# Optimization experiments

Hardware: AMD Instinct MI355X
Metric: run time of the kernel (lower is better)

## Reference

```python
import jax, jax.numpy as jnp
import numpy as np

SP = 4
HEADS = 4
LN_EPS = 1e-4


def _branch(q, k, v, h, hsp, w, wsp, lepe_w, lepe_b, scale, heads):
    # q,k,v: [B, L, Cb] with spatial layout (h hsp w wsp), channel layout (c head)
    B = q.shape[0]
    Cb = q.shape[-1]
    c = Cb // heads

    def win(t):
        t = t.reshape(B, h, hsp, w, wsp, c, heads)
        t = t.transpose(0, 1, 3, 6, 2, 4, 5)  # B,h,w,head,hsp,wsp,c
        return t.reshape(B * h * w, heads, hsp * wsp, c)

    q, k, v = win(q), win(k), win(v)
    Bw = B * h * w
    # LePE: depthwise 3x3 conv on v in image layout [(b h w), (c head), hsp, wsp]
    vimg = v.reshape(Bw, heads, hsp, wsp, c).transpose(0, 4, 1, 2, 3).reshape(Bw, Cb, hsp, wsp)
    lepe = jax.lax.conv_general_dilated(
        vimg, lepe_w, window_strides=(1, 1), padding='SAME',
        dimension_numbers=('NCHW', 'OIHW', 'NCHW'), feature_group_count=Cb)
    lepe = lepe + lepe_b[None, :, None, None]
    lepe = lepe.reshape(Bw, c, heads, hsp, wsp).transpose(0, 2, 3, 4, 1).reshape(Bw, heads, hsp * wsp, c)
    # stripe-window attention
    attn = jax.nn.softmax((q * scale) @ jnp.swapaxes(k, -2, -1), axis=-1)
    o = attn @ v + lepe
    # back to image: [(b h w), head, (hsp wsp), c] -> [B, (c head), (h hsp), (w wsp)]
    o = o.reshape(B, h, w, heads, hsp, wsp, c).transpose(0, 6, 3, 1, 4, 2, 5)
    o = o.reshape(B, Cb, h * hsp, w * wsp)
    return o, attn


def reference(x, ln_g, ln_b, w_qkv, proj_w, proj_b, lepe_w1, lepe_b1, lepe_w2, lepe_b2):
    B, C, H, W = x.shape
    heads, sp = HEADS, SP
    scale = (C // heads) ** (-0.5)  # scale uses full dim // num_heads as in __init__
    # [B,C,H,W] -> [B, H*W, C], LayerNorm over C
    xp = x.transpose(0, 2, 3, 1).reshape(B, H * W, C)
    mu = xp.mean(-1, keepdims=True)
    var = xp.var(-1, keepdims=True)
    xn = (xp - mu) * jax.lax.rsqrt(var + LN_EPS) * ln_g + ln_b
    qkv = xn @ w_qkv.T  # [B, L, 3C]
    q, k, v = jnp.split(qkv, 3, axis=-1)
    Ch = C // 2
    # branch 1: vertical stripes (full H, width sp); branch 2: horizontal stripes
    params = [(1, H, W // sp, sp, lepe_w1, lepe_b1),
              (H // sp, sp, 1, W, lepe_w2, lepe_b2)]
    outs, attns = [], []
    for i, (h, hsp, w, wsp, lw, lb) in enumerate(params):
        sl = slice(i * Ch, (i + 1) * Ch)
        o, a = _branch(q[..., sl], k[..., sl], v[..., sl], h, hsp, w, wsp, lw, lb, scale, heads)
        outs.append(o)
        attns.append(a)
    xcat = jnp.concatenate(outs, axis=1)  # [B, C, H, W]
    out = jnp.einsum('bchw,oc->bohw', xcat, proj_w[:, :, 0, 0]) + proj_b[None, :, None, None]
    return (out, attns[0], attns[1])


def setup_inputs() -> dict:
    key = jax.random.key(0)
    ks = jax.random.split(key, 6)
    B, C, H, W = 8, 256, 64, 64
    return {
        'x': jax.random.normal(ks[0], (B, C, H, W), dtype=jnp.float32),
        'ln_g': jnp.ones((C,), jnp.float32),
        'ln_b': jnp.zeros((C,), jnp.float32),
        'w_qkv': jax.random.normal(ks[1], (3 * C, C), dtype=jnp.float32) * 0.02,
        'proj_w': jax.random.normal(ks[2], (C, C, 1, 1), dtype=jnp.float32) * 0.02,
        'proj_b': jnp.zeros((C,), jnp.float32),
        'lepe_w1': jax.random.normal(ks[3], (C // 2, 1, 3, 3), dtype=jnp.float32) * 0.1,
        'lepe_b1': jnp.zeros((C // 2,), jnp.float32),
        'lepe_w2': jax.random.normal(ks[4], (C // 2, 1, 3, 3), dtype=jnp.float32) * 0.1,
        'lepe_b2': jnp.zeros((C // 2,), jnp.float32),
    }
```

## Files before the change

kernel.cpp:

```cpp
#include <hip/hip_runtime.h>
#include <math.h>

typedef short bf8 __attribute__((ext_vector_type(8)));
typedef float f4  __attribute__((ext_vector_type(4)));

__device__ inline float b2f(unsigned short u) {
    return __uint_as_float(((unsigned int)u) << 16);
}
__device__ inline unsigned short f2b(float f) {
    unsigned int u = __float_as_uint(f);
    u = (u + 0x7fffu + ((u >> 16) & 1u)) >> 16;
    return (unsigned short)u;
}

__global__ __launch_bounds__(256) void k_ln_t(const float* __restrict__ x,
                                              const float* __restrict__ g,
                                              const float* __restrict__ beta,
                                              unsigned short* __restrict__ xnb) {
    __shared__ float xt[32 * 261];
    __shared__ float ps[8][32];
    __shared__ float ps2[8][32];
    __shared__ float ms[32];
    __shared__ float rs[32];
    int l0 = blockIdx.x * 32, b = blockIdx.y;
    int tid = threadIdx.x;
    int tl = tid & 31, c0 = tid >> 5;
    const float* xb = x + (size_t)b * 1048576 + l0 + tl;
    float s = 0.f, s2 = 0.f;
#pragma unroll 8
    for (int rr = 0; rr < 32; ++rr) {
        int c = rr * 8 + c0;
        float v = xb[(size_t)c * 4096];
        int cm = c ^ (((rr >> 2) & 7) << 2);
        xt[tl * 261 + cm] = v;
        s += v; s2 += v * v;
    }
    ps[c0][tl] = s; ps2[c0][tl] = s2;
    __syncthreads();
    if (tid < 32) {
        float t = 0.f, t2 = 0.f;
#pragma unroll
        for (int j = 0; j < 8; ++j) { t += ps[j][tid]; t2 += ps2[j][tid]; }
        float m = t * (1.f / 256.f);
        float var = t2 * (1.f / 256.f) - m * m;
        ms[tid] = m;
        rs[tid] = rsqrtf(var + 1e-4f);
    }
    __syncthreads();
    int lw = tid >> 3, cc = (tid & 7) * 32;
    int xr = (tid & 7) << 2;
    float m = ms[lw], r = rs[lw];
    unsigned short* dst = xnb + ((size_t)b * 4096 + l0 + lw) * 256 + cc;
#pragma unroll
    for (int q4 = 0; q4 < 4; ++q4) {
        int cb = cc + q4 * 8;
        float gv[8], bv[8];
        *(float4*)(gv)     = *(const float4*)(g + cb);
        *(float4*)(gv + 4) = *(const float4*)(g + cb + 4);
        *(float4*)(bv)     = *(const float4*)(beta + cb);
        *(float4*)(bv + 4) = *(const float4*)(beta + cb + 4);
        union { unsigned short u[8]; uint4 v; } pk;
#pragma unroll
        for (int e = 0; e < 8; ++e) {
            int cm = (cb + e) ^ xr;
            pk.u[e] = f2b((xt[lw * 261 + cm] - m) * r * gv[e] + bv[e]);
        }
        *(uint4*)(dst + q4 * 8) = pk.v;
    }
}

__global__ __launch_bounds__(256) void k_wcvt(const float* __restrict__ w,
                                              unsigned short* __restrict__ wb) {
    int i = (blockIdx.x * 256 + threadIdx.x) * 8;
    float4 a = *(const float4*)(w + i);
    float4 c = *(const float4*)(w + i + 4);
    union { unsigned short u[8]; uint4 v; } r;
    r.u[0] = f2b(a.x); r.u[1] = f2b(a.y); r.u[2] = f2b(a.z); r.u[3] = f2b(a.w);
    r.u[4] = f2b(c.x); r.u[5] = f2b(c.y); r.u[6] = f2b(c.z); r.u[7] = f2b(c.w);
    *(uint4*)(wb + i) = r.v;
}

__global__ __launch_bounds__(256) void k_pcvt(const float* __restrict__ pw,
                                              unsigned short* __restrict__ pwb) {
    int idx = blockIdx.x * 256 + threadIdx.x;
    int o = idx >> 8, cp = idx & 255;
    int br = cp >> 7, head = (cp >> 5) & 3, d = cp & 31;
    int c = br * 128 + d * 4 + head;
    pwb[idx] = f2b(pw[o * 256 + c]);
}

__global__ __launch_bounds__(256) void k_qkv(const unsigned short* __restrict__ wb,
                                             const unsigned short* __restrict__ xnb,
                                             unsigned short* __restrict__ qw,
                                             unsigned short* __restrict__ kw,
                                             unsigned short* __restrict__ vw) {
    int jt = blockIdx.x, lt = blockIdx.y, b = blockIdx.z;
    int tid = threadIdx.x;
    int w = tid >> 6, lane = tid & 63;
    int ln15 = lane & 15, quad = lane >> 4;
    const unsigned short* A = wb + (size_t)jt * 64 * 256 + ln15 * 256 + quad * 8;
    const unsigned short* B = xnb + ((size_t)b * 4096 + lt * 256 + w * 64 + ln15) * 256 + quad * 8;
    const f4 z = {0.f, 0.f, 0.f, 0.f};
    f4 acc[4][4];
#pragma unroll
    for (int i = 0; i < 4; i++)
#pragma unroll
        for (int j = 0; j < 4; j++) acc[i][j] = z;
#pragma unroll 2
    for (int k0 = 0; k0 < 256; k0 += 32) {
        bf8 af[4], bvf[4];
#pragma unroll
        for (int i = 0; i < 4; i++) af[i]  = *(const bf8*)(A + i * 16 * 256 + k0);
#pragma unroll
        for (int j = 0; j < 4; j++) bvf[j] = *(const bf8*)(B + j * 16 * 256 + k0);
#pragma unroll
        for (int i = 0; i < 4; i++)
#pragma unroll
            for (int j = 0; j < 4; j++)
                acc[i][j] = __builtin_amdgcn_mfma_f32_16x16x32_bf16(af[i], bvf[j], acc[i][j], 0, 0, 0);
    }
    int lbase = lt * 256 + w * 64;
#pragma unroll
    for (int i = 0; i < 4; i++) {
#pragma unroll
        for (int r = 0; r < 4; r++) {
            int j = jt * 64 + i * 16 + quad * 4 + r;
            int sel = j >> 8;
            int jr = j & 255;
            int branch = jr >> 7;
            int chb = jr & 127;
            int d = chb >> 2, head = chb & 3;
            unsigned short* dst = (sel == 0) ? qw : ((sel == 1) ? kw : vw);
            float sc = (sel == 0) ? 0.125f : 1.f;
#pragma unroll
            for (int jf = 0; jf < 4; jf++) {
                int ll = lbase + jf * 16 + ln15;
                int row = ll >> 6, col = ll & 63;
                int win, pos;
                if (branch == 0) { win = col >> 2; pos = (row << 2) | (col & 3); }
                else             { win = row >> 2; pos = ((row & 3) << 6) | col; }
                int bw = b * 16 + win;
                size_t idx;
                if (sel == 2)
                    idx = ((((size_t)branch * 128 + bw) * 4 + head) * 32 + d) * 256 + pos;
                else
                    idx = ((((size_t)branch * 128 + bw) * 4 + head) * 256 + pos) * 32 + d;
                dst[idx] = f2b(acc[i][jf][r] * sc);
            }
        }
    }
}

__global__ __launch_bounds__(256, 3) void k_attn(const unsigned short* __restrict__ qw,
                                                 const unsigned short* __restrict__ kw,
                                                 const unsigned short* __restrict__ vw,
                                                 const float* __restrict__ lw1,
                                                 const float* __restrict__ lb1,
                                                 const float* __restrict__ lw2,
                                                 const float* __restrict__ lb2,
                                                 float* __restrict__ attn_out,
                                                 unsigned short* __restrict__ xcat) {
    __shared__ __align__(16) char smem[49792];
    float*          olds = (float*)smem;
    unsigned short* vt   = (unsigned short*)(smem + 32896);

    int bid = blockIdx.x;
    int branch = bid >> 9;
    int bw = (bid >> 2) & 127;
    int head = bid & 3;
    int tid = threadIdx.x;
    int w = tid >> 6, lane = tid & 63;
    int ln15 = lane & 15, quad = lane >> 4;
    int rowbase = w * 64;

    size_t base = (((size_t)branch * 128 + bw) * 4 + head) * 8192;
    const unsigned short* qb = qw + base;
    const unsigned short* kb = kw + base;
    const unsigned short* vb = vw + base;

    {
        int d = tid >> 3, ck = (tid & 7) * 32;
        const uint4* s = (const uint4*)(vb + d * 256 + ck);
        uint4* dst = (uint4*)(vt + d * 264 + ck);
        dst[0] = s[0]; dst[1] = s[1]; dst[2] = s[2]; dst[3] = s[3];
    }

    bf8 qf[4];
#pragma unroll
    for (int rt = 0; rt < 4; rt++)
        qf[rt] = *(const bf8*)(qb + (rowbase + rt * 16 + ln15) * 32 + quad * 8);

    const f4 z = {0.f, 0.f, 0.f, 0.f};

    f4 lsum[4] = {z, z, z, z};
    for (int jtile = 0; jtile < 16; jtile++) {
        bf8 kf = *(const bf8*)(kb + (jtile * 16 + ln15) * 32 + quad * 8);
#pragma unroll
        for (int rt = 0; rt < 4; rt++) {
            f4 s = __builtin_amdgcn_mfma_f32_16x16x32_bf16(qf[rt], kf, z, 0, 0, 0);
            lsum[rt].x += __expf(s.x);
            lsum[rt].y += __expf(s.y);
            lsum[rt].z += __expf(s.z);
            lsum[rt].w += __expf(s.w);
        }
    }
    f4 inv[4];
#pragma unroll
    for (int rt = 0; rt < 4; rt++) {
        float a0 = lsum[rt].x, a1 = lsum[rt].y, a2 = lsum[rt].z, a3 = lsum[rt].w;
#pragma unroll
        for (int m = 1; m < 16; m <<= 1) {
            a0 += __shfl_xor(a0, m); a1 += __shfl_xor(a1, m);
            a2 += __shfl_xor(a2, m); a3 += __shfl_xor(a3, m);
        }
        inv[rt].x = 1.f / a0; inv[rt].y = 1.f / a1;
        inv[rt].z = 1.f / a2; inv[rt].w = 1.f / a3;
    }

    __syncthreads();

    unsigned short* plw = ((unsigned short*)olds) + w * 512;
    float* abase = attn_out + (size_t)branch * 33554432ull
                 + ((size_t)(bw * 4 + head)) * 65536;
    f4 oacc[4][2] = {{z, z}, {z, z}, {z, z}, {z, z}};
    for (int t = 0; t < 8; t++) {
        int c0 = t * 32;
        bf8 kf0 = *(const bf8*)(kb + (c0 + ln15) * 32 + quad * 8);
        bf8 kf1 = *(const bf8*)(kb + (c0 + 16 + ln15) * 32 + quad * 8);
        bf8 vf0 = *(const bf8*)(vt + ln15 * 264 + c0 + quad * 8);
        bf8 vf1 = *(const bf8*)(vt + (16 + ln15) * 264 + c0 + quad * 8);
#pragma unroll
        for (int rt = 0; rt < 4; rt++) {
            f4 s0 = __builtin_amdgcn_mfma_f32_16x16x32_bf16(qf[rt], kf0, z, 0, 0, 0);
            f4 s1 = __builtin_amdgcn_mfma_f32_16x16x32_bf16(qf[rt], kf1, z, 0, 0, 0);
            f4 p0, p1;
            p0.x = __expf(s0.x) * inv[rt].x; p0.y = __expf(s0.y) * inv[rt].y;
            p0.z = __expf(s0.z) * inv[rt].z; p0.w = __expf(s0.w) * inv[rt].w;
            p1.x = __expf(s1.x) * inv[rt].x; p1.y = __expf(s1.y) * inv[rt].y;
            p1.z = __expf(s1.z) * inv[rt].z; p1.w = __expf(s1.w) * inv[rt].w;
            float* ar = abase + (size_t)(rowbase + rt * 16 + quad * 4) * 256 + c0 + ln15;
            ar[0]   = p0.x; ar[256] = p0.y; ar[512] = p0.z; ar[768] = p0.w;
            ar[16]  = p1.x; ar[272] = p1.y; ar[528] = p1.z; ar[784] = p1.w;
            plw[(quad * 4 + 0) * 32 + ln15]      = f2b(p0.x);
            plw[(quad * 4 + 1) * 32 + ln15]      = f2b(p0.y);
            plw[(quad * 4 + 2) * 32 + ln15]      = f2b(p0.z);
            plw[(quad * 4 + 3) * 32 + ln15]      = f2b(p0.w);
            plw[(quad * 4 + 0) * 32 + 16 + ln15] = f2b(p1.x);
            plw[(quad * 4 + 1) * 32 + 16 + ln15] = f2b(p1.y);
            plw[(quad * 4 + 2) * 32 + 16 + ln15] = f2b(p1.z);
            plw[(quad * 4 + 3) * 32 + 16 + ln15] = f2b(p1.w);
            bf8 pf = *(const bf8*)(plw + ln15 * 32 + quad * 8);
            oacc[rt][0] = __builtin_amdgcn_mfma_f32_16x16x32_bf16(pf, vf0, oacc[rt][0], 0, 0, 0);
            oacc[rt][1] = __builtin_amdgcn_mfma_f32_16x16x32_bf16(pf, vf1, oacc[rt][1], 0, 0, 0);
        }
    }

    __syncthreads();
#pragma unroll
    for (int rt = 0; rt < 4; rt++)
#pragma unroll
        for (int dt = 0; dt < 2; dt++) {
            int d = dt * 16 + ln15;
            int r = rowbase + rt * 16 + quad * 4;
            olds[d * 257 + r + 0] = oacc[rt][dt][0];
            olds[d * 257 + r + 1] = oacc[rt][dt][1];
            olds[d * 257 + r + 2] = oacc[rt][dt][2];
            olds[d * 257 + r + 3] = oacc[rt][dt][3];
        }
    __syncthreads();

    const float* lw = branch ? lw2 : lw1;
    const float* lb = branch ? lb2 : lb1;
    int p = tid;
    int hs, ws_;
    if (branch == 0) { hs = p >> 2; ws_ = p & 3; }
    else             { hs = p >> 6; ws_ = p & 63; }
    int win = bw & 15, b = bw >> 4;
    int row, col;
    if (branch == 0) { row = p >> 2; col = (win << 2) | (p & 3); }
    else             { row = (win << 2) | (p >> 6); col = p & 63; }
    size_t lpix = (size_t)row * 64 + col;
    unsigned short* xd = xcat + (((size_t)b * 4096 + lpix) * 256) + branch * 128 + head * 32;
#pragma unroll
    for (int dg = 0; dg < 4; ++dg) {
        union { unsigned short u[8]; uint4 v; } pk;
#pragma unroll
        for (int dd = 0; dd < 8; ++dd) {
            int d = dg * 8 + dd;
            float acc = lb[d * 4 + head];
#pragma unroll
            for (int ky = 0; ky < 3; ky++) {
#pragma unroll
                for (int kx = 0; kx < 3; kx++) {
                    int ny = hs + ky - 1, nx = ws_ + kx - 1;
                    bool ok; int np;
                    if (branch == 0) { ok = (ny >= 0 && ny < 64 && nx >= 0 && nx < 4);  np = (ny << 2) | (nx & 3); }
                    else             { ok = (ny >= 0 && ny < 4  && nx >= 0 && nx < 64); np = (ny << 6) | (nx & 63); }
                    if (ok) acc += lw[(d * 4 + head) * 9 + ky * 3 + kx] * b2f(vt[d * 264 + np]);
                }
            }
            pk.u[dd] = f2b(olds[d * 257 + p] + acc);
        }
        *(uint4*)(xd + dg * 8) = pk.v;
    }
}

__global__ __launch_bounds__(256) void k_proj(const unsigned short* __restrict__ pwb,
                                              const float* __restrict__ pb,
                                              const unsigned short* __restrict__ xcat,
                                              float* __restrict__ out) {
    int jt = blockIdx.x, lt = blockIdx.y, b = blockIdx.z;
    int tid = threadIdx.x;
    int w = tid >> 6, lane = tid & 63;
    int ln15 = lane & 15, quad = lane >> 4;
    const unsigned short* A = pwb + (size_t)jt * 64 * 256 + ln15 * 256 + quad * 8;
    const unsigned short* B = xcat + ((size_t)b * 4096 + lt * 256 + w * 64 + ln15) * 256 + quad * 8;
    const f4 z = {0.f, 0.f, 0.f, 0.f};
    f4 acc[4][4];
#pragma unroll
    for (int i = 0; i < 4; i++)
#pragma unroll
        for (int j = 0; j < 4; j++) acc[i][j] = z;
#pragma unroll 2
    for (int k0 = 0; k0 < 256; k0 += 32) {
        bf8 af[4], bvf[4];
#pragma unroll
        for (int i = 0; i < 4; i++) af[i]  = *(const bf8*)(A + i * 16 * 256 + k0);
#pragma unroll
        for (int j = 0; j < 4; j++) bvf[j] = *(const bf8*)(B + j * 16 * 256 + k0);
#pragma unroll
        for (int i = 0; i < 4; i++)
#pragma unroll
            for (int j = 0; j < 4; j++)
                acc[i][j] = __builtin_amdgcn_mfma_f32_16x16x32_bf16(af[i], bvf[j], acc[i][j], 0, 0, 0);
    }
    int lbase = lt * 256 + w * 64;
#pragma unroll
    for (int i = 0; i < 4; i++) {
#pragma unroll
        for (int r = 0; r < 4; r++) {
            int j = jt * 64 + i * 16 + quad * 4 + r;
            float bias = pb[j];
            float* orow = out + ((size_t)b * 256 + j) * 4096;
#pragma unroll
            for (int jf = 0; jf < 4; jf++) {
                int ll = lbase + jf * 16 + ln15;
                orow[ll] = acc[i][jf][r] + bias;
            }
        }
    }
}

extern "C" void kernel_launch(void* const* d_in, const int* in_sizes, int n_in,
                              void* d_out, int out_size, void* d_ws, size_t ws_size,
                              hipStream_t stream) {
    const float* x    = (const float*)d_in[0];
    const float* ln_g = (const float*)d_in[1];
    const float* ln_b = (const float*)d_in[2];
    const float* wqkv = (const float*)d_in[3];
    const float* pw   = (const float*)d_in[4];
    const float* pb   = (const float*)d_in[5];
    const float* lw1  = (const float*)d_in[6];
    const float* lb1  = (const float*)d_in[7];
    const float* lw2  = (const float*)d_in[8];
    const float* lb2  = (const float*)d_in[9];

    float* ws = (float*)d_ws;
    unsigned short* xnb = (unsigned short*)(ws + 65536);
    unsigned short* wb  = xnb + 8388608;
    unsigned short* pwb = wb + 196608;
    unsigned short* qw  = (unsigned short*)(ws + 65536 + 8388608);
    unsigned short* kw  = qw + 8388608;
    unsigned short* vw  = kw + 8388608;
    unsigned short* xcat = xnb;
    float* out  = (float*)d_out;
    float* attn = out + 8388608;

    k_wcvt<<<96, 256, 0, stream>>>(wqkv, wb);
    k_pcvt<<<256, 256, 0, stream>>>(pw, pwb);
    k_ln_t<<<dim3(128, 8), 256, 0, stream>>>(x, ln_g, ln_b, xnb);
    k_qkv<<<dim3(12, 16, 8), 256, 0, stream>>>(wb, xnb, qw, kw, vw);
    k_attn<<<1024, 256, 0, stream>>>(qw, kw, vw, lw1, lb1, lw2, lb2, attn, xcat);
    k_proj<<<dim3(4, 16, 8), 256, 0, stream>>>(pwb, pb, xcat, out);
}
```

Measured before the change: 518.6 us.

## Stage QKV GEMM output in shared memory for coalesced 16-byte window-layout stores

The QKV projection kernel used to write each bf16 result element by element with scattered 2-byte stores into the windowed q/k/v layouts. It now stages the 64x256 output tile in padded shared memory, then gathers 16 contiguous elements per thread and writes them as two uint4 stores per branch and layout. The grid is also reordered so the j-tile is the slowest dimension, which keeps sel, branch and d0 uniform across a block. This adds a barrier, LDS traffic and possible bank conflicts in the gather, in exchange for far fewer and better-coalesced global writes.

```diff
diff --git a/kernel.cpp b/kernel.cpp
--- a/kernel.cpp
+++ b/kernel.cpp
@@ -94,7 +94,8 @@
                                              unsigned short* __restrict__ qw,
                                              unsigned short* __restrict__ kw,
                                              unsigned short* __restrict__ vw) {
-    int jt = blockIdx.x, lt = blockIdx.y, b = blockIdx.z;
+    __shared__ unsigned short sj[64 * 266];
+    int lt = blockIdx.x, b = blockIdx.y, jt = blockIdx.z;
     int tid = threadIdx.x;
     int w = tid >> 6, lane = tid & 63;
     int ln15 = lane & 15, quad = lane >> 4;
@@ -119,33 +120,87 @@
             for (int j = 0; j < 4; j++)
                 acc[i][j] = __builtin_amdgcn_mfma_f32_16x16x32_bf16(af[i], bvf[j], acc[i][j], 0, 0, 0);
     }
-    int lbase = lt * 256 + w * 64;
-#pragma unroll
-    for (int i = 0; i < 4; i++) {
-#pragma unroll
-        for (int r = 0; r < 4; r++) {
-            int j = jt * 64 + i * 16 + quad * 4 + r;
-            int sel = j >> 8;
-            int jr = j & 255;
-            int branch = jr >> 7;
-            int chb = jr & 127;
-            int d = chb >> 2, head = chb & 3;
-            unsigned short* dst = (sel == 0) ? qw : ((sel == 1) ? kw : vw);
-            float sc = (sel == 0) ? 0.125f : 1.f;
-#pragma unroll
-            for (int jf = 0; jf < 4; jf++) {
-                int ll = lbase + jf * 16 + ln15;
-                int row = ll >> 6, col = ll & 63;
-                int win, pos;
-                if (branch == 0) { win = col >> 2; pos = (row << 2) | (col & 3); }
-                else             { win = row >> 2; pos = ((row & 3) << 6) | col; }
-                int bw = b * 16 + win;
-                size_t idx;
-                if (sel == 2)
-                    idx = ((((size_t)branch * 128 + bw) * 4 + head) * 32 + d) * 256 + pos;
-                else
-                    idx = ((((size_t)branch * 128 + bw) * 4 + head) * 256 + pos) * 32 + d;
-                dst[idx] = f2b(acc[i][jf][r] * sc);
+    int sel = jt >> 2;
+    int branch = (jt >> 1) & 1;
+    int d0 = (jt & 1) * 16;
+    float sc = (sel == 0) ? 0.125f : 1.f;
+#pragma unroll
+    for (int i = 0; i < 4; i++)
+#pragma unroll
+        for (int jf = 0; jf < 4; jf++) {
+            int ll = w * 64 + jf * 16 + ln15;
+#pragma unroll
+            for (int r = 0; r < 4; r++)
+                sj[(i * 16 + quad * 4 + r) * 266 + ll] = f2b(acc[i][jf][r] * sc);
+        }
+    __syncthreads();
+
+    if (sel < 2) {
+        unsigned short* dst = (sel == 0) ? qw : kw;
+        if (branch == 0) {
+            int head = tid & 3, win = (tid >> 2) & 15, pgrp = tid >> 6;
+            size_t basewh = (((size_t)b * 16 + win) * 4 + head) * 8192;
+#pragma unroll
+            for (int pp = 0; pp < 4; ++pp) {
+                int posl = pgrp * 4 + pp;
+                int llb = (posl >> 2) * 64 + win * 4 + (posl & 3);
+                union { unsigned short u[16]; uint4 v[2]; } pk;
+#pragma unroll
+                for (int dl = 0; dl < 16; ++dl) {
+                    int jl = (dl >> 2) * 16 + (dl & 3) * 4 + head;
+                    pk.u[dl] = sj[jl * 266 + llb];
+                }
+                unsigned short* o = dst + basewh + (size_t)(lt * 16 + posl) * 32 + d0;
+                *(uint4*)(o)     = pk.v[0];
+                *(uint4*)(o + 8) = pk.v[1];
+            }
+        } else {
+            int head = tid & 3, p16 = tid >> 2;
+            size_t basewh = (((size_t)128 + b * 16 + lt) * 4 + head) * 8192;
+#pragma unroll
+            for (int it = 0; it < 4; ++it) {
+                int pos = p16 + it * 64;
+                union { unsigned short u[16]; uint4 v[2]; } pk;
+#pragma unroll
+                for (int dl = 0; dl < 16; ++dl) {
+                    int jl = (dl >> 2) * 16 + (dl & 3) * 4 + head;
+                    pk.u[dl] = sj[jl * 266 + pos];
+                }
+                unsigned short* o = dst + basewh + (size_t)pos * 32 + d0;
+                *(uint4*)(o)     = pk.v[0];
+                *(uint4*)(o + 8) = pk.v[1];
+            }
+        }
+    } else {
+        if (branch == 0) {
+            int head = tid & 3, win = (tid >> 2) & 15, dgrp = tid >> 6;
+#pragma unroll
+            for (int dd = 0; dd < 4; ++dd) {
+                int dl = dgrp * 4 + dd;
+                int jl = (dl >> 2) * 16 + (dl & 3) * 4 + head;
+                union { unsigned short u[16]; uint4 v[2]; } pk;
+#pragma unroll
+                for (int posl = 0; posl < 16; ++posl) {
+                    int llb = (posl >> 2) * 64 + win * 4 + (posl & 3);
+                    pk.u[posl] = sj[jl * 266 + llb];
+                }
+                unsigned short* o = vw + ((((size_t)b * 16 + win) * 4 + head) * 32 + d0 + dl) * 256 + lt * 16;
+                *(uint4*)(o)     = pk.v[0];
+                *(uint4*)(o + 8) = pk.v[1];
+            }
+        } else {
+            int head = tid & 3, dl = (tid >> 2) & 15, pc = tid >> 6;
+            int jl = (dl >> 2) * 16 + (dl & 3) * 4 + head;
+#pragma unroll
+            for (int it = 0; it < 4; ++it) {
+                int pos0 = pc * 64 + it * 16;
+                union { unsigned short u[16]; uint4 v[2]; } pk;
+#pragma unroll
+                for (int pp = 0; pp < 16; ++pp)
+                    pk.u[pp] = sj[jl * 266 + pos0 + pp];
+                unsigned short* o = vw + ((((size_t)128 + b * 16 + lt) * 4 + head) * 32 + d0 + dl) * 256 + pos0;
+                *(uint4*)(o)     = pk.v[0];
+                *(uint4*)(o + 8) = pk.v[1];
             }
         }
     }
@@ -379,7 +434,7 @@
     k_wcvt<<<96, 256, 0, stream>>>(wqkv, wb);
     k_pcvt<<<256, 256, 0, stream>>>(pw, pwb);
     k_ln_t<<<dim3(128, 8), 256, 0, stream>>>(x, ln_g, ln_b, xnb);
-    k_qkv<<<dim3(12, 16, 8), 256, 0, stream>>>(wb, xnb, qw, kw, vw);
+    k_qkv<<<dim3(16, 8, 12), 256, 0, stream>>>(wb, xnb, qw, kw, vw);
     k_attn<<<1024, 256, 0, stream>>>(qw, kw, vw, lw1, lb1, lw2, lb2, attn, xcat);
     k_proj<<<dim3(4, 16, 8), 256, 0, stream>>>(pwb, pb, xcat, out);
 }
```

New measurement: 505.2 us. -2.6%, faster.
